# Kernel tuning notes

Hardware: AMD Instinct MI355X
Metric: run time of the kernel (lower is better)

The kernel has to match this reference:

```python
import jax, jax.numpy as jnp
import numpy as np

N_NODES = 8192
F_DIM = 64
A_DIM = 8
HID = 32
AVG_DEG = 16.0


def _linear_params(key, fan_in, fan_out):
    # torch nn.Linear default init: U(-1/sqrt(fan_in), 1/sqrt(fan_in))
    s = 1.0 / np.sqrt(fan_in)
    k1, k2 = jax.random.split(key)
    W = jax.random.uniform(k1, (fan_in, fan_out), minval=-s, maxval=s, dtype=jnp.float32)
    b = jax.random.uniform(k2, (fan_out,), minval=-s, maxval=s, dtype=jnp.float32)
    return W, b


def setup_inputs() -> dict:
    key = jax.random.key(0)
    ks = jax.random.split(key, 12)
    N, Fd, Ad, H = N_NODES, F_DIM, A_DIM, HID

    features = jax.random.normal(ks[0], (N, Fd), dtype=jnp.float32)
    # sparse symmetric binary adjacency, zero diagonal (edge weights are discarded
    # by the original code -> all edges weight 1, so binary is the faithful form)
    u = jax.random.uniform(ks[1], (N, N), dtype=jnp.float32)
    adj = (u < AVG_DEG / N).astype(jnp.float32)
    adj = jnp.maximum(adj, adj.T) * (1.0 - jnp.eye(N, dtype=jnp.float32))
    mask = jax.random.uniform(ks[2], (N,), dtype=jnp.float32)  # RL_indice (unused)
    action = jax.random.normal(ks[3], (N, Ad), dtype=jnp.float32)

    We1, be1 = _linear_params(ks[4], Fd + Ad, H)
    We2, be2 = _linear_params(ks[5], H, H)
    Wg, bg = _linear_params(ks[6], H, H)      # GCNConv weight + bias
    Wgd, bgd = _linear_params(ks[7], H, H)    # GraphConv_Dense
    Wp1, bp1 = _linear_params(ks[8], 2 * H, H)
    Wp2, bp2 = _linear_params(ks[9], H, H)
    Wv, bv = _linear_params(ks[10], H, 1)

    return dict(features=features, adjacency=adjacency_fix(adj), mask=mask, action=action,
                We1=We1, be1=be1, We2=We2, be2=be2, Wg=Wg, bg=bg, Wgd=Wgd, bgd=bgd,
                Wp1=Wp1, bp1=bp1, Wp2=Wp2, bp2=bp2, Wv=Wv, bv=bv)


def adjacency_fix(adj):
    return adj


def reference(features, adjacency, mask, action,
              We1, be1, We2, be2, Wg, bg, Wgd, bgd,
              Wp1, bp1, Wp2, bp2, Wv, bv):
    # encoder
    X = jax.nn.relu(jnp.concatenate([features, action], axis=1) @ We1 + be1)  # [N,32]
    X = jax.nn.relu(X @ We2 + be2)                                            # [N,32]

    # GCNConv: out = D^{-1/2} (A + I) D^{-1/2} (X W) + b   (self-loops added, deg incl. self)
    deg = jnp.sum(adjacency, axis=1) + 1.0                 # [N]
    dinv = jax.lax.rsqrt(deg)                              # [N]
    S = (X @ Wg) * dinv[:, None]                           # [N,32] scaled messages
    Xg = (adjacency @ S + S) * dinv[:, None] + bg          # aggregate (A@S) + self-loop (S)
    Xg = jax.nn.relu(Xg)
    Xg = jax.nn.relu(Xg @ Wgd + bgd)

    # policy/value head on [graph || encoder] features
    P = jnp.concatenate([Xg, X], axis=1)                   # [N,64]
    P = jax.nn.relu(P @ Wp1 + bp1)
    P = jax.nn.relu(P @ Wp2 + bp2)
    V = P @ Wv + bv                                        # [N,1]
    return V
```

## Files before the change

kernel.cpp:

```cpp
#include <hip/hip_runtime.h>
#include <math.h>

#define NN 8192
#define FD 64
#define AD 8
#define H  32
#define CAP 128
#define NENC (NN / 256)
#define NPAIR (NN / 2)

typedef unsigned short u16;

#define OW1 0
#define OW2 2304
#define OWG 3328
#define OB1 4352
#define OB2 4384
#define SMEM_FLOATS 4416

__device__ __forceinline__ void scan_row(const float4* __restrict__ arow, const int r,
                                         int* __restrict__ cnt, u16* __restrict__ nbr) {
    int i4 = ((r + 1) >> 2) + (int)threadIdx.x;
    if (i4 >= NN / 4) return;
    float4 v = arow[i4];
    for (;;) {
        const int nx = i4 + 256;
        const bool more = (nx < NN / 4);
        float4 vn;
        if (more) vn = arow[nx];

        const int base = i4 * 4;
        if (v.x != 0.0f && base > r) {
            const int s = atomicAdd(&cnt[r], 1);
            if (s < CAP) nbr[(size_t)r * CAP + s] = (u16)base;
            const int s2 = atomicAdd(&cnt[base], 1);
            if (s2 < CAP) nbr[(size_t)base * CAP + s2] = (u16)r;
        }
        if (v.y != 0.0f && base + 1 > r) {
            const int c = base + 1;
            const int s = atomicAdd(&cnt[r], 1);
            if (s < CAP) nbr[(size_t)r * CAP + s] = (u16)c;
            const int s2 = atomicAdd(&cnt[c], 1);
            if (s2 < CAP) nbr[(size_t)c * CAP + s2] = (u16)r;
        }
        if (v.z != 0.0f && base + 2 > r) {
            const int c = base + 2;
            const int s = atomicAdd(&cnt[r], 1);
            if (s < CAP) nbr[(size_t)r * CAP + s] = (u16)c;
            const int s2 = atomicAdd(&cnt[c], 1);
            if (s2 < CAP) nbr[(size_t)c * CAP + s2] = (u16)r;
        }
        if (v.w != 0.0f && base + 3 > r) {
            const int c = base + 3;
            const int s = atomicAdd(&cnt[r], 1);
            if (s < CAP) nbr[(size_t)r * CAP + s] = (u16)c;
            const int s2 = atomicAdd(&cnt[c], 1);
            if (s2 < CAP) nbr[(size_t)c * CAP + s2] = (u16)r;
        }

        if (!more) break;
        v = vn; i4 = nx;
    }
}

__global__ __launch_bounds__(256, 8) void pre_k(const float4* __restrict__ adj,
                                                const float* __restrict__ feat,
                                                const float* __restrict__ act,
                                                const float* __restrict__ We1,
                                                const float* __restrict__ be1,
                                                const float* __restrict__ We2,
                                                const float* __restrict__ be2,
                                                const float* __restrict__ Wg,
                                                u16* __restrict__ nbr,
                                                int* __restrict__ cnt,
                                                float* __restrict__ X,
                                                float* __restrict__ T) {
    __shared__ float smem[SMEM_FLOATS];

    if (blockIdx.x >= NENC) {
        const int p = blockIdx.x - NENC;
        scan_row(adj + (size_t)p * (NN / 4), p, cnt, nbr);
        const int r2 = NN - 1 - p;
        scan_row(adj + (size_t)r2 * (NN / 4), r2, cnt, nbr);
    } else {
        for (int i = threadIdx.x; i < (FD + AD) * H; i += 256) smem[OW1 + i] = We1[i];
        for (int i = threadIdx.x; i < H * H; i += 256) {
            smem[OW2 + i] = We2[i];
            smem[OWG + i] = Wg[i];
        }
        if (threadIdx.x < H) {
            smem[OB1 + threadIdx.x] = be1[threadIdx.x];
            smem[OB2 + threadIdx.x] = be2[threadIdx.x];
        }
        __syncthreads();

        const int row = blockIdx.x * 256 + threadIdx.x;

        float h1[H];
#pragma unroll
        for (int o = 0; o < H; ++o) h1[o] = smem[OB1 + o];

        const float4* f4 = (const float4*)(feat + (size_t)row * FD);
#pragma unroll
        for (int i = 0; i < FD / 4; ++i) {
            const float4 v = f4[i];
            const int b = 4 * i;
#pragma unroll
            for (int o = 0; o < H; ++o) h1[o] = fmaf(v.x, smem[OW1 + (b + 0) * H + o], h1[o]);
#pragma unroll
            for (int o = 0; o < H; ++o) h1[o] = fmaf(v.y, smem[OW1 + (b + 1) * H + o], h1[o]);
#pragma unroll
            for (int o = 0; o < H; ++o) h1[o] = fmaf(v.z, smem[OW1 + (b + 2) * H + o], h1[o]);
#pragma unroll
            for (int o = 0; o < H; ++o) h1[o] = fmaf(v.w, smem[OW1 + (b + 3) * H + o], h1[o]);
        }
        const float4* a4 = (const float4*)(act + (size_t)row * AD);
#pragma unroll
        for (int i = 0; i < AD / 4; ++i) {
            const float4 v = a4[i];
            const int b = FD + 4 * i;
#pragma unroll
            for (int o = 0; o < H; ++o) h1[o] = fmaf(v.x, smem[OW1 + (b + 0) * H + o], h1[o]);
#pragma unroll
            for (int o = 0; o < H; ++o) h1[o] = fmaf(v.y, smem[OW1 + (b + 1) * H + o], h1[o]);
#pragma unroll
            for (int o = 0; o < H; ++o) h1[o] = fmaf(v.z, smem[OW1 + (b + 2) * H + o], h1[o]);
#pragma unroll
            for (int o = 0; o < H; ++o) h1[o] = fmaf(v.w, smem[OW1 + (b + 3) * H + o], h1[o]);
        }
#pragma unroll
        for (int o = 0; o < H; ++o) h1[o] = fmaxf(h1[o], 0.0f);

        float h2[H];
#pragma unroll
        for (int o = 0; o < H; ++o) h2[o] = smem[OB2 + o];
#pragma unroll
        for (int i = 0; i < H; ++i) {
            const float xi = h1[i];
#pragma unroll
            for (int o = 0; o < H; ++o) h2[o] = fmaf(xi, smem[OW2 + i * H + o], h2[o]);
        }
#pragma unroll
        for (int o = 0; o < H; ++o) h2[o] = fmaxf(h2[o], 0.0f);

        float* Xr = X + (size_t)row * H;
#pragma unroll
        for (int o = 0; o < H; o += 4)
            *(float4*)(Xr + o) = make_float4(h2[o], h2[o + 1], h2[o + 2], h2[o + 3]);

#pragma unroll
        for (int o = 0; o < H; ++o) h1[o] = 0.0f;
#pragma unroll
        for (int i = 0; i < H; ++i) {
            const float xi = h2[i];
#pragma unroll
            for (int o = 0; o < H; ++o) h1[o] = fmaf(xi, smem[OWG + i * H + o], h1[o]);
        }
        float* Tr = T + (size_t)row * H;
#pragma unroll
        for (int o = 0; o < H; o += 4)
            *(float4*)(Tr + o) = make_float4(h1[o], h1[o + 1], h1[o + 2], h1[o + 3]);
    }
}

__global__ __launch_bounds__(64) void fin_k(const float* __restrict__ T,
                                            const float* __restrict__ X,
                                            const u16* __restrict__ nbr,
                                            const int* __restrict__ cnt,
                                            const float* __restrict__ bg,
                                            const float* __restrict__ Wgd,
                                            const float* __restrict__ bgd,
                                            const float* __restrict__ Wp1,
                                            const float* __restrict__ bp1,
                                            const float* __restrict__ Wp2,
                                            const float* __restrict__ bp2,
                                            const float* __restrict__ Wv,
                                            const float* __restrict__ bv,
                                            float* __restrict__ out) {
    __shared__ float sbg[H];
    __shared__ float sWgd[H * H];
    __shared__ float sbgd[H];
    __shared__ float sWp1[2 * H * H];
    __shared__ float sbp1[H];
    __shared__ float sWp2[H * H];
    __shared__ float sbp2[H];
    __shared__ float sWv[H];
    __shared__ float sbv;
    for (int i = threadIdx.x; i < H * H; i += 64) { sWgd[i] = Wgd[i]; sWp2[i] = Wp2[i]; }
    for (int i = threadIdx.x; i < 2 * H * H; i += 64) sWp1[i] = Wp1[i];
    if (threadIdx.x < H) {
        sbg[threadIdx.x]  = bg[threadIdx.x];
        sbgd[threadIdx.x] = bgd[threadIdx.x];
        sbp1[threadIdx.x] = bp1[threadIdx.x];
        sbp2[threadIdx.x] = bp2[threadIdx.x];
        sWv[threadIdx.x]  = Wv[threadIdx.x];
    }
    if (threadIdx.x == 0) sbv = bv[0];
    __syncthreads();

    const int row = blockIdx.x * 64 + threadIdx.x;
    const int n_raw = cnt[row];
    const int n = (n_raw < CAP) ? n_raw : CAP;
    const float di = 1.0f / sqrtf((float)n_raw + 1.0f);

    float acc[H];
    const float4* Tr = (const float4*)(T + (size_t)row * H);
#pragma unroll
    for (int q = 0; q < H / 4; ++q) {
        float4 v = Tr[q];
        acc[4 * q]     = v.x * di; acc[4 * q + 1] = v.y * di;
        acc[4 * q + 2] = v.z * di; acc[4 * q + 3] = v.w * di;
    }

    const u16* myn = nbr + (size_t)row * CAP;
    int e = 0;
    for (; e + 4 <= n; e += 4) {
        const ushort4 ii = *(const ushort4*)(myn + e);
        const int j0 = ii.x, j1 = ii.y, j2 = ii.z, j3 = ii.w;
        const int c0 = cnt[j0], c1 = cnt[j1], c2 = cnt[j2], c3 = cnt[j3];
        const float d0 = 1.0f / sqrtf((float)c0 + 1.0f);
        const float d1 = 1.0f / sqrtf((float)c1 + 1.0f);
        const float d2 = 1.0f / sqrtf((float)c2 + 1.0f);
        const float d3 = 1.0f / sqrtf((float)c3 + 1.0f);
        const float4* T0 = (const float4*)(T + (size_t)j0 * H);
        const float4* T1 = (const float4*)(T + (size_t)j1 * H);
        const float4* T2 = (const float4*)(T + (size_t)j2 * H);
        const float4* T3 = (const float4*)(T + (size_t)j3 * H);
#pragma unroll
        for (int q = 0; q < H / 4; ++q) {
            const float4 a = T0[q], b = T1[q], c = T2[q], d = T3[q];
            acc[4 * q]     = fmaf(a.x, d0, acc[4 * q]);
            acc[4 * q + 1] = fmaf(a.y, d0, acc[4 * q + 1]);
            acc[4 * q + 2] = fmaf(a.z, d0, acc[4 * q + 2]);
            acc[4 * q + 3] = fmaf(a.w, d0, acc[4 * q + 3]);
            acc[4 * q]     = fmaf(b.x, d1, acc[4 * q]);
            acc[4 * q + 1] = fmaf(b.y, d1, acc[4 * q + 1]);
            acc[4 * q + 2] = fmaf(b.z, d1, acc[4 * q + 2]);
            acc[4 * q + 3] = fmaf(b.w, d1, acc[4 * q + 3]);
            acc[4 * q]     = fmaf(c.x, d2, acc[4 * q]);
            acc[4 * q + 1] = fmaf(c.y, d2, acc[4 * q + 1]);
            acc[4 * q + 2] = fmaf(c.z, d2, acc[4 * q + 2]);
            acc[4 * q + 3] = fmaf(c.w, d2, acc[4 * q + 3]);
            acc[4 * q]     = fmaf(d.x, d3, acc[4 * q]);
            acc[4 * q + 1] = fmaf(d.y, d3, acc[4 * q + 1]);
            acc[4 * q + 2] = fmaf(d.z, d3, acc[4 * q + 2]);
            acc[4 * q + 3] = fmaf(d.w, d3, acc[4 * q + 3]);
        }
    }
    for (; e < n; ++e) {
        const int j = myn[e];
        const int cj = cnt[j];
        const float dj = 1.0f / sqrtf((float)cj + 1.0f);
        const float4* Tj = (const float4*)(T + (size_t)j * H);
#pragma unroll
        for (int q = 0; q < H / 4; ++q) {
            const float4 v = Tj[q];
            acc[4 * q]     = fmaf(v.x, dj, acc[4 * q]);
            acc[4 * q + 1] = fmaf(v.y, dj, acc[4 * q + 1]);
            acc[4 * q + 2] = fmaf(v.z, dj, acc[4 * q + 2]);
            acc[4 * q + 3] = fmaf(v.w, dj, acc[4 * q + 3]);
        }
    }

    float xg[H];
#pragma unroll
    for (int k = 0; k < H; ++k) xg[k] = fmaxf(fmaf(acc[k], di, sbg[k]), 0.0f);

    float xg2[H];
#pragma unroll
    for (int o = 0; o < H; ++o) xg2[o] = sbgd[o];
#pragma unroll
    for (int k = 0; k < H; ++k) {
        const float xk = xg[k];
#pragma unroll
        for (int o = 0; o < H; ++o) xg2[o] = fmaf(xk, sWgd[k * H + o], xg2[o]);
    }
#pragma unroll
    for (int o = 0; o < H; ++o) xg2[o] = fmaxf(xg2[o], 0.0f);

    float x[H];
    const float4* Xr = (const float4*)(X + (size_t)row * H);
#pragma unroll
    for (int q = 0; q < H / 4; ++q) {
        float4 v = Xr[q];
        x[4 * q] = v.x; x[4 * q + 1] = v.y; x[4 * q + 2] = v.z; x[4 * q + 3] = v.w;
    }

    float p1[H];
#pragma unroll
    for (int o = 0; o < H; ++o) p1[o] = sbp1[o];
#pragma unroll
    for (int k = 0; k < H; ++k) {
        const float xk = xg2[k];
#pragma unroll
        for (int o = 0; o < H; ++o) p1[o] = fmaf(xk, sWp1[k * H + o], p1[o]);
    }
#pragma unroll
    for (int k = 0; k < H; ++k) {
        const float xk = x[k];
#pragma unroll
        for (int o = 0; o < H; ++o) p1[o] = fmaf(xk, sWp1[(H + k) * H + o], p1[o]);
    }
#pragma unroll
    for (int o = 0; o < H; ++o) p1[o] = fmaxf(p1[o], 0.0f);

    float p2[H];
#pragma unroll
    for (int o = 0; o < H; ++o) p2[o] = sbp2[o];
#pragma unroll
    for (int k = 0; k < H; ++k) {
        const float xk = p1[k];
#pragma unroll
        for (int o = 0; o < H; ++o) p2[o] = fmaf(xk, sWp2[k * H + o], p2[o]);
    }

    float v = sbv;
#pragma unroll
    for (int k = 0; k < H; ++k) v = fmaf(fmaxf(p2[k], 0.0f), sWv[k], v);

    out[row] = v;
}

extern "C" void kernel_launch(void* const* d_in, const int* in_sizes, int n_in,
                              void* d_out, int out_size, void* d_ws, size_t ws_size,
                              hipStream_t stream) {
    (void)in_sizes; (void)n_in; (void)out_size; (void)ws_size;

    const float* feat = (const float*)d_in[0];
    const float* adj  = (const float*)d_in[1];
    const float* act  = (const float*)d_in[3];
    const float* We1  = (const float*)d_in[4];
    const float* be1  = (const float*)d_in[5];
    const float* We2  = (const float*)d_in[6];
    const float* be2  = (const float*)d_in[7];
    const float* Wg   = (const float*)d_in[8];
    const float* bg   = (const float*)d_in[9];
    const float* Wgd  = (const float*)d_in[10];
    const float* bgd  = (const float*)d_in[11];
    const float* Wp1  = (const float*)d_in[12];
    const float* bp1  = (const float*)d_in[13];
    const float* Wp2  = (const float*)d_in[14];
    const float* bp2  = (const float*)d_in[15];
    const float* Wv   = (const float*)d_in[16];
    const float* bv   = (const float*)d_in[17];

    char* ws = (char*)d_ws;
    u16*   nbr  = (u16*)ws;
    char*  p    = ws + (size_t)NN * CAP * sizeof(u16);
    int*   cnt  = (int*)p;            p += (size_t)NN * 4;
    float* X    = (float*)p;          p += (size_t)NN * H * 4;
    float* T    = (float*)p;

    float* out = (float*)d_out;

    hipMemsetAsync(cnt, 0, (size_t)NN * sizeof(int), stream);
    pre_k<<<NENC + NPAIR, 256, 0, stream>>>((const float4*)adj, feat, act,
                                            We1, be1, We2, be2, Wg,
                                            nbr, cnt, X, T);
    fin_k<<<NN / 64, 64, 0, stream>>>(T, X, nbr, cnt, bg, Wgd, bgd,
                                      Wp1, bp1, Wp2, bp2, Wv, bv, out);
}
```

Baseline: 431.6 us.

## Split neighbor lists into upper/lower halves with LDS row counters and batched adjacency loads

The adjacency scan now keeps the two rows a block owns in LDS counters, so the upper-triangle neighbor list is filled without global atomics on the row counter. Mirrored (lower) entries go to a separate list and counter. The block also issues all of its float4 loads for both rows up front (9 per thread) before processing them, which raises memory-level parallelism. This removes contention on hot global atomics and lengthens the adjacency stream in flight. The costs are more registers (occupancy hint lowered to 4), twice the neighbor-list workspace, and two gather passes per row in the final kernel.

```diff
diff --git a/kernel.cpp b/kernel.cpp
--- a/kernel.cpp
+++ b/kernel.cpp
@@ -18,52 +18,7 @@
 #define OB2 4384
 #define SMEM_FLOATS 4416
 
-__device__ __forceinline__ void scan_row(const float4* __restrict__ arow, const int r,
-                                         int* __restrict__ cnt, u16* __restrict__ nbr) {
-    int i4 = ((r + 1) >> 2) + (int)threadIdx.x;
-    if (i4 >= NN / 4) return;
-    float4 v = arow[i4];
-    for (;;) {
-        const int nx = i4 + 256;
-        const bool more = (nx < NN / 4);
-        float4 vn;
-        if (more) vn = arow[nx];
-
-        const int base = i4 * 4;
-        if (v.x != 0.0f && base > r) {
-            const int s = atomicAdd(&cnt[r], 1);
-            if (s < CAP) nbr[(size_t)r * CAP + s] = (u16)base;
-            const int s2 = atomicAdd(&cnt[base], 1);
-            if (s2 < CAP) nbr[(size_t)base * CAP + s2] = (u16)r;
-        }
-        if (v.y != 0.0f && base + 1 > r) {
-            const int c = base + 1;
-            const int s = atomicAdd(&cnt[r], 1);
-            if (s < CAP) nbr[(size_t)r * CAP + s] = (u16)c;
-            const int s2 = atomicAdd(&cnt[c], 1);
-            if (s2 < CAP) nbr[(size_t)c * CAP + s2] = (u16)r;
-        }
-        if (v.z != 0.0f && base + 2 > r) {
-            const int c = base + 2;
-            const int s = atomicAdd(&cnt[r], 1);
-            if (s < CAP) nbr[(size_t)r * CAP + s] = (u16)c;
-            const int s2 = atomicAdd(&cnt[c], 1);
-            if (s2 < CAP) nbr[(size_t)c * CAP + s2] = (u16)r;
-        }
-        if (v.w != 0.0f && base + 3 > r) {
-            const int c = base + 3;
-            const int s = atomicAdd(&cnt[r], 1);
-            if (s < CAP) nbr[(size_t)r * CAP + s] = (u16)c;
-            const int s2 = atomicAdd(&cnt[c], 1);
-            if (s2 < CAP) nbr[(size_t)c * CAP + s2] = (u16)r;
-        }
-
-        if (!more) break;
-        v = vn; i4 = nx;
-    }
-}
-
-__global__ __launch_bounds__(256, 8) void pre_k(const float4* __restrict__ adj,
+__global__ __launch_bounds__(256, 4) void pre_k(const float4* __restrict__ adj,
                                                 const float* __restrict__ feat,
                                                 const float* __restrict__ act,
                                                 const float* __restrict__ We1,
@@ -71,17 +26,68 @@
                                                 const float* __restrict__ We2,
                                                 const float* __restrict__ be2,
                                                 const float* __restrict__ Wg,
-                                                u16* __restrict__ nbr,
-                                                int* __restrict__ cnt,
+                                                u16* __restrict__ nbrU,
+                                                u16* __restrict__ nbrL,
+                                                int* __restrict__ cntU,
+                                                int* __restrict__ cntL,
                                                 float* __restrict__ X,
                                                 float* __restrict__ T) {
     __shared__ float smem[SMEM_FLOATS];
+    __shared__ int sPQ[2];
 
     if (blockIdx.x >= NENC) {
-        const int p = blockIdx.x - NENC;
-        scan_row(adj + (size_t)p * (NN / 4), p, cnt, nbr);
-        const int r2 = NN - 1 - p;
-        scan_row(adj + (size_t)r2 * (NN / 4), r2, cnt, nbr);
+        const int p  = blockIdx.x - NENC;
+        const int q  = NN - 1 - p;
+        const int s0 = (p + 1) >> 2;
+        const int l0 = NN / 4 - s0;
+        const int s1 = (q + 1) >> 2;
+        const int l1 = NN / 4 - s1;
+        const int total = l0 + l1;
+
+        if (threadIdx.x == 0) { sPQ[0] = 0; sPQ[1] = 0; }
+        __syncthreads();
+
+        const int tid = (int)threadIdx.x;
+
+        float4 v[9];
+#pragma unroll
+        for (int s = 0; s < 9; ++s) {
+            const int vi = s * 256 + tid;
+            if (vi < total) {
+                const bool inP = vi < l0;
+                const int r  = inP ? p : q;
+                const int i4 = inP ? (s0 + vi) : (s1 + (vi - l0));
+                v[s] = adj[(size_t)r * (NN / 4) + i4];
+            }
+        }
+
+#pragma unroll
+        for (int s = 0; s < 9; ++s) {
+            const int vi = s * 256 + tid;
+            if (vi >= total) continue;
+            const bool inP = vi < l0;
+            const int r    = inP ? p : q;
+            const int idx  = inP ? 0 : 1;
+            const int i4   = inP ? (s0 + vi) : (s1 + (vi - l0));
+            const int base = i4 * 4;
+            const float4 vv = v[s];
+#pragma unroll
+            for (int k = 0; k < 4; ++k) {
+                const float val = (k == 0) ? vv.x : (k == 1) ? vv.y : (k == 2) ? vv.z : vv.w;
+                const int c = base + k;
+                if (val != 0.0f && c > r) {
+                    const int sl = atomicAdd(&sPQ[idx], 1);
+                    if (sl < CAP) nbrU[(size_t)r * CAP + sl] = (u16)c;
+                    const int s2 = atomicAdd(&cntL[c], 1);
+                    if (s2 < CAP) nbrL[(size_t)c * CAP + s2] = (u16)r;
+                }
+            }
+        }
+        __syncthreads();
+        if (threadIdx.x == 0) {
+            cntU[p] = sPQ[0];
+            cntU[q] = sPQ[1];
+        }
     } else {
         for (int i = threadIdx.x; i < (FD + AD) * H; i += 256) smem[OW1 + i] = We1[i];
         for (int i = threadIdx.x; i < H * H; i += 256) {
@@ -163,10 +169,65 @@
     }
 }
 
+__device__ __forceinline__ void gather_list(const float* __restrict__ T,
+                                            const u16* __restrict__ list, const int n,
+                                            const int* __restrict__ cntU,
+                                            const int* __restrict__ cntL,
+                                            float acc[H]) {
+    int e = 0;
+    for (; e + 4 <= n; e += 4) {
+        const ushort4 ii = *(const ushort4*)(list + e);
+        const int j0 = ii.x, j1 = ii.y, j2 = ii.z, j3 = ii.w;
+        const float d0 = 1.0f / sqrtf((float)(cntU[j0] + cntL[j0]) + 1.0f);
+        const float d1 = 1.0f / sqrtf((float)(cntU[j1] + cntL[j1]) + 1.0f);
+        const float d2 = 1.0f / sqrtf((float)(cntU[j2] + cntL[j2]) + 1.0f);
+        const float d3 = 1.0f / sqrtf((float)(cntU[j3] + cntL[j3]) + 1.0f);
+        const float4* T0 = (const float4*)(T + (size_t)j0 * H);
+        const float4* T1 = (const float4*)(T + (size_t)j1 * H);
+        const float4* T2 = (const float4*)(T + (size_t)j2 * H);
+        const float4* T3 = (const float4*)(T + (size_t)j3 * H);
+#pragma unroll
+        for (int q = 0; q < H / 4; ++q) {
+            const float4 a = T0[q], b = T1[q], c = T2[q], d = T3[q];
+            acc[4 * q]     = fmaf(a.x, d0, acc[4 * q]);
+            acc[4 * q + 1] = fmaf(a.y, d0, acc[4 * q + 1]);
+            acc[4 * q + 2] = fmaf(a.z, d0, acc[4 * q + 2]);
+            acc[4 * q + 3] = fmaf(a.w, d0, acc[4 * q + 3]);
+            acc[4 * q]     = fmaf(b.x, d1, acc[4 * q]);
+            acc[4 * q + 1] = fmaf(b.y, d1, acc[4 * q + 1]);
+            acc[4 * q + 2] = fmaf(b.z, d1, acc[4 * q + 2]);
+            acc[4 * q + 3] = fmaf(b.w, d1, acc[4 * q + 3]);
+            acc[4 * q]     = fmaf(c.x, d2, acc[4 * q]);
+            acc[4 * q + 1] = fmaf(c.y, d2, acc[4 * q + 1]);
+            acc[4 * q + 2] = fmaf(c.z, d2, acc[4 * q + 2]);
+            acc[4 * q + 3] = fmaf(c.w, d2, acc[4 * q + 3]);
+            acc[4 * q]     = fmaf(d.x, d3, acc[4 * q]);
+            acc[4 * q + 1] = fmaf(d.y, d3, acc[4 * q + 1]);
+            acc[4 * q + 2] = fmaf(d.z, d3, acc[4 * q + 2]);
+            acc[4 * q + 3] = fmaf(d.w, d3, acc[4 * q + 3]);
+        }
+    }
+    for (; e < n; ++e) {
+        const int j = list[e];
+        const float dj = 1.0f / sqrtf((float)(cntU[j] + cntL[j]) + 1.0f);
+        const float4* Tj = (const float4*)(T + (size_t)j * H);
+#pragma unroll
+        for (int q = 0; q < H / 4; ++q) {
+            const float4 v = Tj[q];
+            acc[4 * q]     = fmaf(v.x, dj, acc[4 * q]);
+            acc[4 * q + 1] = fmaf(v.y, dj, acc[4 * q + 1]);
+            acc[4 * q + 2] = fmaf(v.z, dj, acc[4 * q + 2]);
+            acc[4 * q + 3] = fmaf(v.w, dj, acc[4 * q + 3]);
+        }
+    }
+}
+
 __global__ __launch_bounds__(64) void fin_k(const float* __restrict__ T,
                                             const float* __restrict__ X,
-                                            const u16* __restrict__ nbr,
-                                            const int* __restrict__ cnt,
+                                            const u16* __restrict__ nbrU,
+                                            const u16* __restrict__ nbrL,
+                                            const int* __restrict__ cntU,
+                                            const int* __restrict__ cntL,
                                             const float* __restrict__ bg,
                                             const float* __restrict__ Wgd,
                                             const float* __restrict__ bgd,
@@ -199,9 +260,10 @@
     __syncthreads();
 
     const int row = blockIdx.x * 64 + threadIdx.x;
-    const int n_raw = cnt[row];
-    const int n = (n_raw < CAP) ? n_raw : CAP;
-    const float di = 1.0f / sqrtf((float)n_raw + 1.0f);
+    const int cu = cntU[row], cl = cntL[row];
+    const int nu = (cu < CAP) ? cu : CAP;
+    const int nl = (cl < CAP) ? cl : CAP;
+    const float di = 1.0f / sqrtf((float)(cu + cl) + 1.0f);
 
     float acc[H];
     const float4* Tr = (const float4*)(T + (size_t)row * H);
@@ -212,55 +274,8 @@
         acc[4 * q + 2] = v.z * di; acc[4 * q + 3] = v.w * di;
     }
 
-    const u16* myn = nbr + (size_t)row * CAP;
-    int e = 0;
-    for (; e + 4 <= n; e += 4) {
-        const ushort4 ii = *(const ushort4*)(myn + e);
-        const int j0 = ii.x, j1 = ii.y, j2 = ii.z, j3 = ii.w;
-        const int c0 = cnt[j0], c1 = cnt[j1], c2 = cnt[j2], c3 = cnt[j3];
-        const float d0 = 1.0f / sqrtf((float)c0 + 1.0f);
-        const float d1 = 1.0f / sqrtf((float)c1 + 1.0f);
-        const float d2 = 1.0f / sqrtf((float)c2 + 1.0f);
-        const float d3 = 1.0f / sqrtf((float)c3 + 1.0f);
-        const float4* T0 = (const float4*)(T + (size_t)j0 * H);
-        const float4* T1 = (const float4*)(T + (size_t)j1 * H);
-        const float4* T2 = (const float4*)(T + (size_t)j2 * H);
-        const float4* T3 = (const float4*)(T + (size_t)j3 * H);
-#pragma unroll
-        for (int q = 0; q < H / 4; ++q) {
-            const float4 a = T0[q], b = T1[q], c = T2[q], d = T3[q];
-            acc[4 * q]     = fmaf(a.x, d0, acc[4 * q]);
-            acc[4 * q + 1] = fmaf(a.y, d0, acc[4 * q + 1]);
-            acc[4 * q + 2] = fmaf(a.z, d0, acc[4 * q + 2]);
-            acc[4 * q + 3] = fmaf(a.w, d0, acc[4 * q + 3]);
-            acc[4 * q]     = fmaf(b.x, d1, acc[4 * q]);
-            acc[4 * q + 1] = fmaf(b.y, d1, acc[4 * q + 1]);
-            acc[4 * q + 2] = fmaf(b.z, d1, acc[4 * q + 2]);
-            acc[4 * q + 3] = fmaf(b.w, d1, acc[4 * q + 3]);
-            acc[4 * q]     = fmaf(c.x, d2, acc[4 * q]);
-            acc[4 * q + 1] = fmaf(c.y, d2, acc[4 * q + 1]);
-            acc[4 * q + 2] = fmaf(c.z, d2, acc[4 * q + 2]);
-            acc[4 * q + 3] = fmaf(c.w, d2, acc[4 * q + 3]);
-            acc[4 * q]     = fmaf(d.x, d3, acc[4 * q]);
-            acc[4 * q + 1] = fmaf(d.y, d3, acc[4 * q + 1]);
-            acc[4 * q + 2] = fmaf(d.z, d3, acc[4 * q + 2]);
-            acc[4 * q + 3] = fmaf(d.w, d3, acc[4 * q + 3]);
-        }
-    }
-    for (; e < n; ++e) {
-        const int j = myn[e];
-        const int cj = cnt[j];
-        const float dj = 1.0f / sqrtf((float)cj + 1.0f);
-        const float4* Tj = (const float4*)(T + (size_t)j * H);
-#pragma unroll
-        for (int q = 0; q < H / 4; ++q) {
-            const float4 v = Tj[q];
-            acc[4 * q]     = fmaf(v.x, dj, acc[4 * q]);
-            acc[4 * q + 1] = fmaf(v.y, dj, acc[4 * q + 1]);
-            acc[4 * q + 2] = fmaf(v.z, dj, acc[4 * q + 2]);
-            acc[4 * q + 3] = fmaf(v.w, dj, acc[4 * q + 3]);
-        }
-    }
+    gather_list(T, nbrU + (size_t)row * CAP, nu, cntU, cntL, acc);
+    gather_list(T, nbrL + (size_t)row * CAP, nl, cntU, cntL, acc);
 
     float xg[H];
 #pragma unroll
@@ -345,18 +360,20 @@
     const float* bv   = (const float*)d_in[17];
 
     char* ws = (char*)d_ws;
-    u16*   nbr  = (u16*)ws;
-    char*  p    = ws + (size_t)NN * CAP * sizeof(u16);
-    int*   cnt  = (int*)p;            p += (size_t)NN * 4;
+    u16*   nbrU = (u16*)ws;
+    u16*   nbrL = (u16*)(ws + (size_t)NN * CAP * 2);
+    char*  p    = ws + 2 * (size_t)NN * CAP * 2;
+    int*   cntU = (int*)p;            p += (size_t)NN * 4;
+    int*   cntL = (int*)p;            p += (size_t)NN * 4;
     float* X    = (float*)p;          p += (size_t)NN * H * 4;
     float* T    = (float*)p;
 
     float* out = (float*)d_out;
 
-    hipMemsetAsync(cnt, 0, (size_t)NN * sizeof(int), stream);
+    hipMemsetAsync(cntU, 0, 2 * (size_t)NN * sizeof(int), stream);
     pre_k<<<NENC + NPAIR, 256, 0, stream>>>((const float4*)adj, feat, act,
                                             We1, be1, We2, be2, Wg,
-                                            nbr, cnt, X, T);
-    fin_k<<<NN / 64, 64, 0, stream>>>(T, X, nbr, cnt, bg, Wgd, bgd,
+                                            nbrU, nbrL, cntU, cntL, X, T);
+    fin_k<<<NN / 64, 64, 0, stream>>>(T, X, nbrU, nbrL, cntU, cntL, bg, Wgd, bgd,
                                       Wp1, bp1, Wp2, bp2, Wv, bv, out);
 }
```

Measured after the change: 430.2 us. About the same (-0.3%).
